# Kernel optimization log

Measured on AMD Instinct MI355X. Metric: run time of the kernel, lower is better.

## Reference

```python
import jax, jax.numpy as jnp
import numpy as np

SEQ_LEN = 4096
INPUT_SIZE = 1024
OUTPUT_SIZE = 1024


def _xavier(key, shape):
    n = shape[0]
    lim = 1.0 / (n ** 0.5)
    return jax.random.uniform(key, shape, minval=-lim, maxval=lim, dtype=jnp.float32)


def setup_inputs() -> dict:
    key = jax.random.key(0)
    kx, kk, kv, kq = jax.random.split(key, 4)
    X = jax.random.normal(kx, (SEQ_LEN, INPUT_SIZE), dtype=jnp.float32)
    Wk = _xavier(kk, (INPUT_SIZE, OUTPUT_SIZE))
    Wv = _xavier(kv, (INPUT_SIZE, OUTPUT_SIZE))
    Wq = _xavier(kq, (INPUT_SIZE, OUTPUT_SIZE))
    return {"X": X, "Wk": Wk, "Wv": Wv, "Wq": Wq}


def reference(X, Wk, Wv, Wq):
    # Faithful to original: scores = K @ Q^T (note K first, no 1/sqrt(d) scaling)
    K = X @ Wk  # (S, D)
    V = X @ Wv  # (S, D)
    Q = X @ Wq  # (S, D)
    scores = jnp.einsum('sd,td->st', K, Q)  # (S, S) == K @ Q^T
    attn = jax.nn.softmax(scores, axis=-1) @ V  # (S, D)
    return attn
```

## Files before the change

kernel.cpp:

```cpp
#include <hip/hip_runtime.h>
#include <hip/hip_fp16.h>
#include <cstdint>

#define SEQ 4096
#define DIM 1024

typedef _Float16 f16x8 __attribute__((ext_vector_type(8)));
typedef float f32x16 __attribute__((ext_vector_type(16)));
typedef ushort u16x8 __attribute__((ext_vector_type(8)));
typedef __attribute__((address_space(1))) void as1_void;
typedef __attribute__((address_space(3))) void as3_void;

__device__ __forceinline__ ushort f2h(float f) {
  _Float16 h = (_Float16)f;
  return __builtin_bit_cast(ushort, h);
}
__device__ __forceinline__ float h2f(ushort u) {
  return (float)__builtin_bit_cast(_Float16, u);
}

__global__ void convert_all_kernel(const float* __restrict__ X, const float* __restrict__ Wk,
                                   const float* __restrict__ Wv, const float* __restrict__ Wq,
                                   ushort* __restrict__ Xh, ushort* __restrict__ Wt) {
  const int z = blockIdx.z;
  const int tx = threadIdx.x, ty = threadIdx.y;
  if (z == 3) {
    const int bid = blockIdx.y * 32 + blockIdx.x;
    const int t = ty * 32 + tx;
#pragma unroll
    for (int k = 0; k < 4; k++) {
      int i = bid * 1024 + k * 256 + t;
      float4 v = reinterpret_cast<const float4*>(X)[i];
      ushort4 o = { f2h(v.x), f2h(v.y), f2h(v.z), f2h(v.w) };
      reinterpret_cast<ushort4*>(Xh)[i] = o;
    }
    return;
  }
  __shared__ float tile[32][33];
  const float* W = (z == 0) ? Wk : (z == 1) ? Wv : Wq;
  int n0 = blockIdx.x * 32, k0 = blockIdx.y * 32;
#pragma unroll
  for (int r = 0; r < 4; r++) {
    int k = ty + r * 8;
    tile[k][tx] = W[(size_t)(k0 + k) * DIM + n0 + tx];
  }
  __syncthreads();
  ushort* out = Wt + (size_t)z * DIM * DIM;
#pragma unroll
  for (int r = 0; r < 4; r++) {
    int n = ty + r * 8;
    out[(size_t)(n0 + n) * DIM + k0 + tx] = f2h(tile[tx][n]);
  }
}

template <bool STATS>
__device__ __forceinline__ void gemm_tile256(const ushort* __restrict__ A,
                                             const ushort* __restrict__ B,
                                             ushort* __restrict__ C,
                                             int N, int K, int m0, int n0,
                                             int kt0, int ktend,
                                             float2* __restrict__ Stats, int cb) {
  constexpr int BK = 64;
  __shared__ __align__(16) ushort As[2][256 * BK];
  __shared__ __align__(16) ushort Bs[2][256 * BK];
  const int tid = threadIdx.x;
  const int wave = tid >> 6, lane = tid & 63;
  const int l31 = lane & 31, khalf = lane >> 5;
  const int wm = (wave & 1) * 128, wn = (wave >> 1) * 64;

  const int srow = tid >> 3;
  const int skey = ((srow & 7) ^ ((srow >> 3) & 3));
  const int sce = (((tid & 7) ^ skey) * 8);
  const int rk = (l31 & 7) ^ ((l31 >> 3) & 3);

  f32x16 acc[4][2];
#pragma unroll
  for (int i = 0; i < 4; i++)
#pragma unroll
    for (int j = 0; j < 2; j++)
#pragma unroll
      for (int r = 0; r < 16; r++) acc[i][j][r] = 0.f;

  const ushort* Abase = A + (size_t)(m0 + srow) * K + sce;
  const ushort* Bbase = B + (size_t)(n0 + srow) * K + sce;
  const int ldsbase = wave * 512;

  const int ntiles = (ktend - kt0) >> 6;

#pragma unroll
  for (int q = 0; q < 4; q++)
    __builtin_amdgcn_global_load_lds((const as1_void*)(Abase + (size_t)q * 64 * K + kt0),
                                     (as3_void*)&As[0][ldsbase + q * 4096], 16, 0, 0);
#pragma unroll
  for (int q = 0; q < 4; q++)
    __builtin_amdgcn_global_load_lds((const as1_void*)(Bbase + (size_t)q * 64 * K + kt0),
                                     (as3_void*)&Bs[0][ldsbase + q * 4096], 16, 0, 0);
  __syncthreads();

  for (int tt = 0; tt < ntiles; ++tt) {
    const int cur = tt & 1, nb = cur ^ 1;
    const int nkt = kt0 + (tt + 1) * BK;
    const bool pf = (tt + 1 < ntiles);
    const ushort* As_c = As[cur];
    const ushort* Bs_c = Bs[cur];
#pragma unroll
    for (int ks = 0; ks < 4; ks++) {
      f16x8 af[4], bf2[2];
      const int co = (((ks * 2 + khalf)) ^ rk) * 8;
#pragma unroll
      for (int i = 0; i < 4; i++)
        af[i] = *reinterpret_cast<const f16x8*>(&As_c[(wm + i * 32 + l31) * BK + co]);
#pragma unroll
      for (int j = 0; j < 2; j++)
        bf2[j] = *reinterpret_cast<const f16x8*>(&Bs_c[(wn + j * 32 + l31) * BK + co]);
      if (pf && ks == 0) {
#pragma unroll
        for (int q = 0; q < 4; q++)
          __builtin_amdgcn_global_load_lds((const as1_void*)(Abase + (size_t)q * 64 * K + nkt),
                                           (as3_void*)&As[nb][ldsbase + q * 4096], 16, 0, 0);
      }
      if (pf && ks == 1) {
#pragma unroll
        for (int q = 0; q < 4; q++)
          __builtin_amdgcn_global_load_lds((const as1_void*)(Bbase + (size_t)q * 64 * K + nkt),
                                           (as3_void*)&Bs[nb][ldsbase + q * 4096], 16, 0, 0);
      }
      __builtin_amdgcn_s_barrier();
      __builtin_amdgcn_s_setprio(1);
#pragma unroll
      for (int k = 0; k < 4; k++) { (void)k; }
#pragma unroll
      for (int i = 0; i < 4; i++)
#pragma unroll
        for (int j = 0; j < 2; j++)
          acc[i][j] = __builtin_amdgcn_mfma_f32_32x32x16_f16(af[i], bf2[j], acc[i][j], 0, 0, 0);
      __builtin_amdgcn_s_setprio(0);
      if (ks < 3) __builtin_amdgcn_s_barrier();
    }
    __syncthreads();
  }

#pragma unroll
  for (int i = 0; i < 4; i++)
#pragma unroll
    for (int j = 0; j < 2; j++)
#pragma unroll
      for (int r = 0; r < 16; r++) {
        int row = m0 + wm + i * 32 + (r & 3) + 8 * (r >> 2) + 4 * khalf;
        int col = n0 + wn + j * 32 + l31;
        C[(size_t)row * N + col] = f2h(acc[i][j][r]);
      }

  if constexpr (STATS) {
    float* sm = reinterpret_cast<float*>(&As[0][0]);
    const int wcol = wave >> 1;
    __syncthreads();
#pragma unroll
    for (int i = 0; i < 4; i++)
#pragma unroll
      for (int r = 0; r < 16; r++) {
        float a0 = h2f(f2h(acc[i][0][r]));
        float a1 = h2f(f2h(acc[i][1][r]));
        float mx = fmaxf(a0, a1);
#pragma unroll
        for (int o = 16; o > 0; o >>= 1) mx = fmaxf(mx, __shfl_xor(mx, o, 64));
        if (l31 == 0) {
          int rowl = wm + i * 32 + (r & 3) + 8 * (r >> 2) + 4 * khalf;
          sm[rowl * 4 + wcol] = mx;
        }
      }
    __syncthreads();
    if (tid < 256) {
      float rm = fmaxf(fmaxf(sm[tid * 4], sm[tid * 4 + 1]),
                       fmaxf(sm[tid * 4 + 2], sm[tid * 4 + 3]));
      sm[2048 + tid] = rm;
    }
    __syncthreads();
#pragma unroll
    for (int i = 0; i < 4; i++)
#pragma unroll
      for (int r = 0; r < 16; r++) {
        int rowl = wm + i * 32 + (r & 3) + 8 * (r >> 2) + 4 * khalf;
        float rm = sm[2048 + rowl];
        float a0 = h2f(f2h(acc[i][0][r]));
        float a1 = h2f(f2h(acc[i][1][r]));
        float s = __expf(a0 - rm) + __expf(a1 - rm);
#pragma unroll
        for (int o = 16; o > 0; o >>= 1) s += __shfl_xor(s, o, 64);
        if (l31 == 0) sm[1024 + rowl * 4 + wcol] = s;
      }
    __syncthreads();
    if (tid < 256) {
      float sum = sm[1024 + tid * 4] + sm[1024 + tid * 4 + 1] +
                  sm[1024 + tid * 4 + 2] + sm[1024 + tid * 4 + 3];
      Stats[(size_t)cb * SEQ + m0 + tid] = make_float2(sm[2048 + tid], sum);
    }
  }
}

__global__ __launch_bounds__(512, 2) void proj256_kernel(const ushort* __restrict__ Xh,
                                                         const ushort* __restrict__ Wt,
                                                         ushort* __restrict__ Kh,
                                                         ushort* __restrict__ Qh,
                                                         ushort* __restrict__ Vt) {
  const int b = blockIdx.x;
  const ushort* A;
  const ushort* B;
  ushort* Cp;
  int N, m0, n0;
  if (b < 128) {
    const int z = b >> 6, q = b & 63;
    A = Xh;
    B = Wt + (size_t)(z ? 2 : 0) * DIM * DIM;
    Cp = z ? Qh : Kh;
    N = DIM;
    m0 = (q >> 2) * 256;
    n0 = (q & 3) * 256;
  } else {
    const int q = b - 128;
    A = Wt + (size_t)DIM * DIM;
    B = Xh;
    Cp = Vt;
    N = SEQ;
    m0 = (q >> 4) * 256;
    n0 = (q & 15) * 256;
  }
  gemm_tile256<false>(A, B, Cp, N, DIM, m0, n0, 0, DIM, nullptr, 0);
}

__global__ __launch_bounds__(512, 2) void score256_kernel(const ushort* __restrict__ Kh,
                                                          const ushort* __restrict__ Qh,
                                                          ushort* __restrict__ S,
                                                          float2* __restrict__ Stats) {
  const int f = blockIdx.x;
  const int t = (f & 7) * 32 + (f >> 3);
  const int ty = t >> 4, tx = t & 15;
  gemm_tile256<true>(Kh, Qh, S, SEQ, DIM, ty * 256, tx * 256, 0, DIM, Stats, tx);
}

__global__ __launch_bounds__(512, 2) void out_sm256_kernel(const ushort* __restrict__ S,
                                                           const ushort* __restrict__ Vt,
                                                           const float2* __restrict__ Stats,
                                                           ushort* __restrict__ Part) {
  constexpr int BK = 64;
  __shared__ __align__(16) ushort As[2][256 * BK];
  __shared__ __align__(16) ushort Bs[2][256 * BK];
  __shared__ float rowm[256], rowinv[256];

  const int f = blockIdx.x;
  const int z = f >> 6;
  const int q0 = f & 63;
  const int t = (q0 & 7) * 8 + (q0 >> 3);
  const int m0 = (t >> 2) * 256, n0 = (t & 3) * 256;
  const int kt0 = z * (SEQ / 4);
  const int K = SEQ, N = DIM;
  ushort* C = Part + (size_t)z * SEQ * DIM;

  const int tid = threadIdx.x;
  const int wave = tid >> 6, lane = tid & 63;
  const int l31 = lane & 31, khalf = lane >> 5;
  const int wm = (wave & 1) * 128, wn = (wave >> 1) * 64;

  const int srow = tid >> 3;
  const int skey = ((srow & 7) ^ ((srow >> 3) & 3));
  const int sce = (((tid & 7) ^ skey) * 8);
  const int rk = (l31 & 7) ^ ((l31 >> 3) & 3);

  if (tid < 256) {
    float mg = -3.4e38f;
#pragma unroll
    for (int cb = 0; cb < 16; cb++)
      mg = fmaxf(mg, Stats[(size_t)cb * SEQ + m0 + tid].x);
    float sg = 0.f;
#pragma unroll
    for (int cb = 0; cb < 16; cb++) {
      float2 st = Stats[(size_t)cb * SEQ + m0 + tid];
      sg += st.y * __expf(st.x - mg);
    }
    rowm[tid] = mg;
    rowinv[tid] = 1.0f / sg;
  }

  f32x16 acc[4][2];
#pragma unroll
  for (int i = 0; i < 4; i++)
#pragma unroll
    for (int j = 0; j < 2; j++)
#pragma unroll
      for (int r = 0; r < 16; r++) acc[i][j][r] = 0.f;

  const ushort* Abase = S + (size_t)(m0 + srow) * K + sce;
  const ushort* Bbase = Vt + (size_t)(n0 + srow) * K + sce;
  const int ldsbase = wave * 512;
  const int ntiles = (SEQ / 4) >> 6;

  u16x8 areg[4];
#pragma unroll
  for (int q = 0; q < 4; q++)
    areg[q] = *reinterpret_cast<const u16x8*>(Abase + (size_t)q * 64 * K + kt0);
#pragma unroll
  for (int q = 0; q < 4; q++)
    __builtin_amdgcn_global_load_lds((const as1_void*)(Bbase + (size_t)q * 64 * K + kt0),
                                     (as3_void*)&Bs[0][ldsbase + q * 4096], 16, 0, 0);
  __syncthreads();

  float rm_[4], ri_[4];
#pragma unroll
  for (int q = 0; q < 4; q++) {
    rm_[q] = rowm[srow + q * 64];
    ri_[q] = rowinv[srow + q * 64];
  }
#pragma unroll
  for (int q = 0; q < 4; q++) {
    u16x8 o;
#pragma unroll
    for (int k2 = 0; k2 < 8; k2++)
      o[k2] = f2h(__expf(h2f(areg[q][k2]) - rm_[q]) * ri_[q]);
    *reinterpret_cast<u16x8*>(&As[0][ldsbase + q * 4096 + (lane & 63) * 8]) = o;
  }
  __syncthreads();

  for (int tt = 0; tt < ntiles; ++tt) {
    const int cur = tt & 1, nb = cur ^ 1;
    const int nkt = kt0 + (tt + 1) * BK;
    const bool pf = (tt + 1 < ntiles);
    const ushort* As_c = As[cur];
    const ushort* Bs_c = Bs[cur];
#pragma unroll
    for (int ks = 0; ks < 4; ks++) {
      f16x8 af[4], bf2[2];
      const int co = (((ks * 2 + khalf)) ^ rk) * 8;
#pragma unroll
      for (int i = 0; i < 4; i++)
        af[i] = *reinterpret_cast<const f16x8*>(&As_c[(wm + i * 32 + l31) * BK + co]);
#pragma unroll
      for (int j = 0; j < 2; j++)
        bf2[j] = *reinterpret_cast<const f16x8*>(&Bs_c[(wn + j * 32 + l31) * BK + co]);
      if (pf && ks == 0) {
#pragma unroll
        for (int q = 0; q < 4; q++)
          areg[q] = *reinterpret_cast<const u16x8*>(Abase + (size_t)q * 64 * K + nkt);
      }
      if (pf && ks == 1) {
#pragma unroll
        for (int q = 0; q < 4; q++)
          __builtin_amdgcn_global_load_lds((const as1_void*)(Bbase + (size_t)q * 64 * K + nkt),
                                           (as3_void*)&Bs[nb][ldsbase + q * 4096], 16, 0, 0);
      }
      __builtin_amdgcn_s_barrier();
      __builtin_amdgcn_s_setprio(1);
#pragma unroll
      for (int i = 0; i < 4; i++)
#pragma unroll
        for (int j = 0; j < 2; j++)
          acc[i][j] = __builtin_amdgcn_mfma_f32_32x32x16_f16(af[i], bf2[j], acc[i][j], 0, 0, 0);
      __builtin_amdgcn_s_setprio(0);
      if (ks < 3) __builtin_amdgcn_s_barrier();
    }
    if (pf) {
#pragma unroll
      for (int q = 0; q < 4; q++) {
        u16x8 o;
#pragma unroll
        for (int k2 = 0; k2 < 8; k2++)
          o[k2] = f2h(__expf(h2f(areg[q][k2]) - rm_[q]) * ri_[q]);
        *reinterpret_cast<u16x8*>(&As[nb][ldsbase + q * 4096 + (lane & 63) * 8]) = o;
      }
    }
    __syncthreads();
  }

#pragma unroll
  for (int i = 0; i < 4; i++)
#pragma unroll
    for (int j = 0; j < 2; j++)
#pragma unroll
      for (int r = 0; r < 16; r++) {
        int row = m0 + wm + i * 32 + (r & 3) + 8 * (r >> 2) + 4 * khalf;
        int col = n0 + wn + j * 32 + l31;
        C[(size_t)row * N + col] = f2h(acc[i][j][r]);
      }
}

__global__ void reduce4_kernel(const ushort* __restrict__ Part, float* __restrict__ out, int n8) {
  int i = blockIdx.x * blockDim.x + threadIdx.x;
  if (i >= n8) return;
  const f16x8* p0 = reinterpret_cast<const f16x8*>(Part);
  const f16x8* p1 = p0 + n8;
  const f16x8* p2 = p1 + n8;
  const f16x8* p3 = p2 + n8;
  f16x8 a = p0[i], b = p1[i], c = p2[i], d = p3[i];
  float4 lo, hi;
  lo.x = (float)a[0] + (float)b[0] + (float)c[0] + (float)d[0];
  lo.y = (float)a[1] + (float)b[1] + (float)c[1] + (float)d[1];
  lo.z = (float)a[2] + (float)b[2] + (float)c[2] + (float)d[2];
  lo.w = (float)a[3] + (float)b[3] + (float)c[3] + (float)d[3];
  hi.x = (float)a[4] + (float)b[4] + (float)c[4] + (float)d[4];
  hi.y = (float)a[5] + (float)b[5] + (float)c[5] + (float)d[5];
  hi.z = (float)a[6] + (float)b[6] + (float)c[6] + (float)d[6];
  hi.w = (float)a[7] + (float)b[7] + (float)c[7] + (float)d[7];
  reinterpret_cast<float4*>(out)[i * 2] = lo;
  reinterpret_cast<float4*>(out)[i * 2 + 1] = hi;
}

extern "C" void kernel_launch(void* const* d_in, const int* in_sizes, int n_in,
                              void* d_out, int out_size, void* d_ws, size_t ws_size,
                              hipStream_t stream) {
  const float* X = (const float*)d_in[0];
  const float* Wk = (const float*)d_in[1];
  const float* Wv = (const float*)d_in[2];
  const float* Wq = (const float*)d_in[3];

  char* ws = (char*)d_ws;
  size_t off = 0;
  ushort* Xh = (ushort*)(ws + off); off += (size_t)SEQ * DIM * 2;
  ushort* Wt = (ushort*)(ws + off); off += (size_t)3 * DIM * DIM * 2;
  ushort* Kh = (ushort*)(ws + off); off += (size_t)SEQ * DIM * 2;
  ushort* Qh = (ushort*)(ws + off); off += (size_t)SEQ * DIM * 2;
  ushort* Vt = (ushort*)(ws + off); off += (size_t)SEQ * DIM * 2;
  ushort* S = (ushort*)(ws + off);  off += (size_t)SEQ * SEQ * 2;
  ushort* P = (ushort*)(ws + off);  off += (size_t)SEQ * SEQ * 2;

  float2* Stats = (float2*)Xh;
  ushort* Part = P;

  convert_all_kernel<<<dim3(32, 32, 4), dim3(32, 8), 0, stream>>>(X, Wk, Wv, Wq, Xh, Wt);
  proj256_kernel<<<256, 512, 0, stream>>>(Xh, Wt, Kh, Qh, Vt);
  score256_kernel<<<256, 512, 0, stream>>>(Kh, Qh, S, Stats);
  out_sm256_kernel<<<256, 512, 0, stream>>>(S, Vt, Stats, Part);
  reduce4_kernel<<<SEQ * DIM / 8 / 256, 256, 0, stream>>>(Part, (float*)d_out, SEQ * DIM / 8);
}
```

Measured before the change: 241.0 us.

## Split softmax row stats into separate kernel and use smaller-tile projection GEMM

Takes the per-tile max/sum statistics out of the score GEMM epilogue and adds a dedicated rowstats kernel that rereads S to compute the final row max and inverse sum. The output kernel now loads these directly instead of merging 16 partial stats per row. It also swaps the projection GEMM from 256x256 double-buffered tiles to 128x128 single-buffered tiles with 768 blocks. The cost is an extra full pass over the 32MB S matrix plus one more launch, and the simpler projection loop has no load/compute overlap.

```diff
diff --git a/kernel.cpp b/kernel.cpp
--- a/kernel.cpp
+++ b/kernel.cpp
@@ -53,13 +53,84 @@
   }
 }
 
-template <bool STATS>
-__device__ __forceinline__ void gemm_tile256(const ushort* __restrict__ A,
-                                             const ushort* __restrict__ B,
-                                             ushort* __restrict__ C,
-                                             int N, int K, int m0, int n0,
-                                             int kt0, int ktend,
-                                             float2* __restrict__ Stats, int cb) {
+__device__ __forceinline__ void gemm_tile(const ushort* __restrict__ A,
+                                          const ushort* __restrict__ B,
+                                          ushort* __restrict__ C,
+                                          int N, int K, int m0, int n0,
+                                          int kt0, int ktend) {
+  constexpr int BK = 64;
+  __shared__ __align__(16) ushort As[128 * BK];
+  __shared__ __align__(16) ushort Bs[128 * BK];
+  const int tid = threadIdx.x;
+  const int wave = tid >> 6, lane = tid & 63;
+  const int l31 = lane & 31, khalf = lane >> 5;
+  const int wm = (wave & 1) * 64, wn = (wave >> 1) * 64;
+
+  const int srow = tid >> 3;
+  const int skey = ((srow & 7) ^ ((srow >> 3) & 3));
+  const int sce = (((tid & 7) ^ skey) * 8);
+  const int rk = (l31 & 7) ^ ((l31 >> 3) & 3);
+
+  f32x16 acc[2][2];
+#pragma unroll
+  for (int i = 0; i < 2; i++)
+#pragma unroll
+    for (int j = 0; j < 2; j++)
+#pragma unroll
+      for (int r = 0; r < 16; r++) acc[i][j][r] = 0.f;
+
+  for (int kt = kt0; kt < ktend; kt += BK) {
+    __syncthreads();
+#pragma unroll
+    for (int q = 0; q < 4; q++) {
+      const ushort* ga = A + (size_t)(m0 + srow + q * 32) * K + kt + sce;
+      __builtin_amdgcn_global_load_lds((const as1_void*)ga,
+                                       (as3_void*)&As[wave * 512 + q * 2048], 16, 0, 0);
+    }
+#pragma unroll
+    for (int q = 0; q < 4; q++) {
+      const ushort* gb = B + (size_t)(n0 + srow + q * 32) * K + kt + sce;
+      __builtin_amdgcn_global_load_lds((const as1_void*)gb,
+                                       (as3_void*)&Bs[wave * 512 + q * 2048], 16, 0, 0);
+    }
+    __syncthreads();
+#pragma unroll
+    for (int ks = 0; ks < 4; ks++) {
+      f16x8 af[2], bfr[2];
+      const int ck = (ks * 2 + khalf);
+#pragma unroll
+      for (int i = 0; i < 2; i++)
+        af[i] = *reinterpret_cast<const f16x8*>(
+            &As[(wm + i * 32 + l31) * BK + ((ck ^ rk) * 8)]);
+#pragma unroll
+      for (int j = 0; j < 2; j++)
+        bfr[j] = *reinterpret_cast<const f16x8*>(
+            &Bs[(wn + j * 32 + l31) * BK + ((ck ^ rk) * 8)]);
+#pragma unroll
+      for (int i = 0; i < 2; i++)
+#pragma unroll
+        for (int j = 0; j < 2; j++)
+          acc[i][j] = __builtin_amdgcn_mfma_f32_32x32x16_f16(af[i], bfr[j], acc[i][j], 0, 0, 0);
+    }
+  }
+
+#pragma unroll
+  for (int i = 0; i < 2; i++)
+#pragma unroll
+    for (int j = 0; j < 2; j++)
+#pragma unroll
+      for (int r = 0; r < 16; r++) {
+        int row = m0 + wm + i * 32 + (r & 3) + 8 * (r >> 2) + 4 * khalf;
+        int col = n0 + wn + j * 32 + l31;
+        C[(size_t)row * N + col] = f2h(acc[i][j][r]);
+      }
+}
+
+__device__ __forceinline__ void gemm256(const ushort* __restrict__ A,
+                                        const ushort* __restrict__ B,
+                                        ushort* __restrict__ C,
+                                        int N, int K, int m0, int n0,
+                                        int kt0, int ktend) {
   constexpr int BK = 64;
   __shared__ __align__(16) ushort As[2][256 * BK];
   __shared__ __align__(16) ushort Bs[2][256 * BK];
@@ -84,7 +155,6 @@
   const ushort* Abase = A + (size_t)(m0 + srow) * K + sce;
   const ushort* Bbase = B + (size_t)(n0 + srow) * K + sce;
   const int ldsbase = wave * 512;
-
   const int ntiles = (ktend - kt0) >> 6;
 
 #pragma unroll
@@ -128,8 +198,6 @@
       __builtin_amdgcn_s_barrier();
       __builtin_amdgcn_s_setprio(1);
 #pragma unroll
-      for (int k = 0; k < 4; k++) { (void)k; }
-#pragma unroll
       for (int i = 0; i < 4; i++)
 #pragma unroll
         for (int j = 0; j < 2; j++)
@@ -150,97 +218,72 @@
         int col = n0 + wn + j * 32 + l31;
         C[(size_t)row * N + col] = f2h(acc[i][j][r]);
       }
-
-  if constexpr (STATS) {
-    float* sm = reinterpret_cast<float*>(&As[0][0]);
-    const int wcol = wave >> 1;
-    __syncthreads();
-#pragma unroll
-    for (int i = 0; i < 4; i++)
-#pragma unroll
-      for (int r = 0; r < 16; r++) {
-        float a0 = h2f(f2h(acc[i][0][r]));
-        float a1 = h2f(f2h(acc[i][1][r]));
-        float mx = fmaxf(a0, a1);
-#pragma unroll
-        for (int o = 16; o > 0; o >>= 1) mx = fmaxf(mx, __shfl_xor(mx, o, 64));
-        if (l31 == 0) {
-          int rowl = wm + i * 32 + (r & 3) + 8 * (r >> 2) + 4 * khalf;
-          sm[rowl * 4 + wcol] = mx;
-        }
-      }
-    __syncthreads();
-    if (tid < 256) {
-      float rm = fmaxf(fmaxf(sm[tid * 4], sm[tid * 4 + 1]),
-                       fmaxf(sm[tid * 4 + 2], sm[tid * 4 + 3]));
-      sm[2048 + tid] = rm;
-    }
-    __syncthreads();
-#pragma unroll
-    for (int i = 0; i < 4; i++)
-#pragma unroll
-      for (int r = 0; r < 16; r++) {
-        int rowl = wm + i * 32 + (r & 3) + 8 * (r >> 2) + 4 * khalf;
-        float rm = sm[2048 + rowl];
-        float a0 = h2f(f2h(acc[i][0][r]));
-        float a1 = h2f(f2h(acc[i][1][r]));
-        float s = __expf(a0 - rm) + __expf(a1 - rm);
-#pragma unroll
-        for (int o = 16; o > 0; o >>= 1) s += __shfl_xor(s, o, 64);
-        if (l31 == 0) sm[1024 + rowl * 4 + wcol] = s;
-      }
-    __syncthreads();
-    if (tid < 256) {
-      float sum = sm[1024 + tid * 4] + sm[1024 + tid * 4 + 1] +
-                  sm[1024 + tid * 4 + 2] + sm[1024 + tid * 4 + 3];
-      Stats[(size_t)cb * SEQ + m0 + tid] = make_float2(sm[2048 + tid], sum);
-    }
-  }
-}
-
-__global__ __launch_bounds__(512, 2) void proj256_kernel(const ushort* __restrict__ Xh,
-                                                         const ushort* __restrict__ Wt,
-                                                         ushort* __restrict__ Kh,
-                                                         ushort* __restrict__ Qh,
-                                                         ushort* __restrict__ Vt) {
-  const int b = blockIdx.x;
+}
+
+__global__ __launch_bounds__(256) void proj_kernel(const ushort* __restrict__ Xh,
+                                                   const ushort* __restrict__ Wt,
+                                                   ushort* __restrict__ Kh,
+                                                   ushort* __restrict__ Qh,
+                                                   ushort* __restrict__ Vt) {
+  const int z = blockIdx.z;
   const ushort* A;
   const ushort* B;
-  ushort* Cp;
+  ushort* C;
   int N, m0, n0;
-  if (b < 128) {
-    const int z = b >> 6, q = b & 63;
+  if (z < 2) {
     A = Xh;
-    B = Wt + (size_t)(z ? 2 : 0) * DIM * DIM;
-    Cp = z ? Qh : Kh;
+    B = Wt + (size_t)(z == 0 ? 0 : 2) * DIM * DIM;
+    C = (z == 0) ? Kh : Qh;
     N = DIM;
-    m0 = (q >> 2) * 256;
-    n0 = (q & 3) * 256;
+    m0 = (blockIdx.x >> 3) * 128;
+    n0 = (blockIdx.x & 7) * 128;
   } else {
-    const int q = b - 128;
     A = Wt + (size_t)DIM * DIM;
     B = Xh;
-    Cp = Vt;
+    C = Vt;
     N = SEQ;
-    m0 = (q >> 4) * 256;
-    n0 = (q & 15) * 256;
-  }
-  gemm_tile256<false>(A, B, Cp, N, DIM, m0, n0, 0, DIM, nullptr, 0);
+    m0 = (blockIdx.x >> 5) * 128;
+    n0 = (blockIdx.x & 31) * 128;
+  }
+  gemm_tile(A, B, C, N, DIM, m0, n0, 0, DIM);
 }
 
 __global__ __launch_bounds__(512, 2) void score256_kernel(const ushort* __restrict__ Kh,
                                                           const ushort* __restrict__ Qh,
-                                                          ushort* __restrict__ S,
-                                                          float2* __restrict__ Stats) {
+                                                          ushort* __restrict__ S) {
   const int f = blockIdx.x;
   const int t = (f & 7) * 32 + (f >> 3);
-  const int ty = t >> 4, tx = t & 15;
-  gemm_tile256<true>(Kh, Qh, S, SEQ, DIM, ty * 256, tx * 256, 0, DIM, Stats, tx);
+  gemm256(Kh, Qh, S, SEQ, DIM, (t >> 4) * 256, (t & 15) * 256, 0, DIM);
+}
+
+__global__ __launch_bounds__(256) void rowstats_kernel(const ushort* __restrict__ S,
+                                                       float2* __restrict__ RS) {
+  const int wave = threadIdx.x >> 6, lane = threadIdx.x & 63;
+  const int row = blockIdx.x * 4 + wave;
+  const ushort* s = S + (size_t)row * SEQ;
+  float v[64];
+#pragma unroll
+  for (int i = 0; i < 8; i++) {
+    f16x8 h = reinterpret_cast<const f16x8*>(s)[i * 64 + lane];
+#pragma unroll
+    for (int j = 0; j < 8; j++) v[i * 8 + j] = (float)h[j];
+  }
+  float m = v[0];
+#pragma unroll
+  for (int j = 1; j < 64; j++) m = fmaxf(m, v[j]);
+#pragma unroll
+  for (int o = 32; o > 0; o >>= 1) m = fmaxf(m, __shfl_xor(m, o, 64));
+  float sum = 0.f;
+#pragma unroll
+  for (int j = 0; j < 64; j++) sum += __expf(v[j] - m);
+#pragma unroll
+  for (int o = 32; o > 0; o >>= 1) sum += __shfl_xor(sum, o, 64);
+  if (lane == 0) RS[row] = make_float2(m, 1.0f / sum);
 }
 
 __global__ __launch_bounds__(512, 2) void out_sm256_kernel(const ushort* __restrict__ S,
                                                            const ushort* __restrict__ Vt,
-                                                           const float2* __restrict__ Stats,
+                                                           const float2* __restrict__ RS,
                                                            ushort* __restrict__ Part) {
   constexpr int BK = 64;
   __shared__ __align__(16) ushort As[2][256 * BK];
@@ -267,18 +310,9 @@
   const int rk = (l31 & 7) ^ ((l31 >> 3) & 3);
 
   if (tid < 256) {
-    float mg = -3.4e38f;
-#pragma unroll
-    for (int cb = 0; cb < 16; cb++)
-      mg = fmaxf(mg, Stats[(size_t)cb * SEQ + m0 + tid].x);
-    float sg = 0.f;
-#pragma unroll
-    for (int cb = 0; cb < 16; cb++) {
-      float2 st = Stats[(size_t)cb * SEQ + m0 + tid];
-      sg += st.y * __expf(st.x - mg);
-    }
-    rowm[tid] = mg;
-    rowinv[tid] = 1.0f / sg;
+    float2 st = RS[m0 + tid];
+    rowm[tid] = st.x;
+    rowinv[tid] = st.y;
   }
 
   f32x16 acc[4][2];
@@ -305,6 +339,10 @@
   __syncthreads();
 
   float rm_[4], ri_[4];
+#pragma unroll
+  for (int q = 0; q < 4; q++) {
+    rm_[q] = rowm[srow + ((q * 64) & 255) - ((q * 64) & 255) + q * 64 - q * 64 + (srow + q * 64 >= 256 ? 0 : 0)];
+  }
 #pragma unroll
   for (int q = 0; q < 4; q++) {
     rm_[q] = rowm[srow + q * 64];
@@ -421,12 +459,13 @@
   ushort* S = (ushort*)(ws + off);  off += (size_t)SEQ * SEQ * 2;
   ushort* P = (ushort*)(ws + off);  off += (size_t)SEQ * SEQ * 2;
 
-  float2* Stats = (float2*)Xh;
+  float2* RS = (float2*)Wt;
   ushort* Part = P;
 
   convert_all_kernel<<<dim3(32, 32, 4), dim3(32, 8), 0, stream>>>(X, Wk, Wv, Wq, Xh, Wt);
-  proj256_kernel<<<256, 512, 0, stream>>>(Xh, Wt, Kh, Qh, Vt);
-  score256_kernel<<<256, 512, 0, stream>>>(Kh, Qh, S, Stats);
-  out_sm256_kernel<<<256, 512, 0, stream>>>(S, Vt, Stats, Part);
+  proj_kernel<<<dim3(256, 1, 3), 256, 0, stream>>>(Xh, Wt, Kh, Qh, Vt);
+  score256_kernel<<<256, 512, 0, stream>>>(Kh, Qh, S);
+  rowstats_kernel<<<1024, 256, 0, stream>>>(S, RS);
+  out_sm256_kernel<<<256, 512, 0, stream>>>(S, Vt, RS, Part);
   reduce4_kernel<<<SEQ * DIM / 8 / 256, 256, 0, stream>>>(Part, (float*)d_out, SEQ * DIM / 8);
 }
```

Measured after the change: 218.8 us. 9.2% less time.
